# Optimization experiments

Measured on AMD Instinct MI355X. Metric: run time of the kernel, lower is better.

Reference implementation:

```python
import jax, jax.numpy as jnp
import numpy as np

N_NODES = 10000
N_EDGES = 640000
D_IN = 128
D_OUT = 128


def setup_inputs() -> dict:
    key = jax.random.key(0)
    k1, k2, k3, k4 = jax.random.split(key, 4)
    x = jax.random.normal(k1, (N_NODES, D_IN), dtype=jnp.float32)
    # PyG GCNConv weight: [dim_out, dim_in] (glorot)
    W = jax.random.normal(k2, (D_OUT, D_IN), dtype=jnp.float32) * (1.0 / np.sqrt(D_IN))
    b = jnp.zeros((D_OUT,), dtype=jnp.float32)
    edge_weight = jax.random.uniform(k3, (N_EDGES,), dtype=jnp.float32)
    edge_index = jax.random.randint(k4, (2, N_EDGES), 0, N_NODES, dtype=jnp.int32)
    return {"x": x, "W": W, "b": b, "edge_weight": edge_weight, "edge_index": edge_index}


def reference(x, W, b, edge_weight, edge_index):
    N = x.shape[0]
    # --- add self loops (fill weight = 1.0), PyG default ---
    loops = jnp.arange(N, dtype=edge_index.dtype)
    src = jnp.concatenate([edge_index[0], loops])
    dst = jnp.concatenate([edge_index[1], loops])
    ew = jnp.concatenate([edge_weight, jnp.ones((N,), dtype=edge_weight.dtype)])
    # --- symmetric GCN normalization: deg from target index ---
    deg = jax.ops.segment_sum(ew, dst, num_segments=N)
    dinv = jnp.where(deg > 0, jax.lax.rsqrt(deg), 0.0)
    norm = dinv[src] * ew * dinv[dst]  # [E+N]
    # --- linear transform then gather-scale-scatter aggregation ---
    h = x @ W.T  # [N, D_OUT]
    msgs = h[src] * norm[:, None]  # [E+N, D_OUT]
    out = jax.ops.segment_sum(msgs, dst, num_segments=N)
    return out + b
```

## Files before the change

kernel.cpp:

```cpp
#include <hip/hip_runtime.h>

#define N_NODES 10000
#define N_EDGES 640000
#define D 128
#define CAP 128

typedef unsigned long long ull;
typedef unsigned short u16;
typedef unsigned int u32;

#define CHUNKS 128
#define EPC 5000
#define GEMM_NPB 32
#define GEMM_BLOCKS ((N_NODES + GEMM_NPB - 1) / GEMM_NPB)
#define SMEM_BYTES 80000
#define FRACM 0xffffffffffffull

__device__ __forceinline__ u16 f2bf(float f) {
    unsigned u = __float_as_uint(f);
    unsigned r = (u + 0x7fffu + ((u >> 16) & 1u)) >> 16;
    return (u16)r;
}


__global__ void __launch_bounds__(256, 2) k_hist_fill_gemm(
    const int* __restrict__ src, const int* __restrict__ dst,
    const float* __restrict__ ew, ull* __restrict__ gpacked,
    const float* __restrict__ x, const float* __restrict__ W,
    u16* __restrict__ h_bf, ull* __restrict__ csr)
{
    extern __shared__ char smem[];
    const int t = threadIdx.x;

    if (blockIdx.x < CHUNKS) {
        ull* hist = (ull*)smem;
        for (int i = t; i < N_NODES; i += 256) hist[i] = 0;
        __syncthreads();

        const int e0 = blockIdx.x * EPC;
        u32 dlr[20];
        #pragma unroll
        for (int i = 0; i < 20; ++i) {
            int idx = i * 256 + t;
            dlr[i] = 0xffffffffu;
            if (idx < EPC) {
                int e = e0 + idx;
                int d = dst[e];
                ull add = (1ull << 48) | (ull)(ew[e] * 4294967296.0f);
                ull old = atomicAdd(&hist[d], add);
                dlr[i] = ((u32)d << 7) | (u32)((old >> 48) & 127u);
            }
        }
        __syncthreads();

        for (int i = t; i < N_NODES; i += 256) {
            ull v = hist[i];
            if (v) {
                ull old = atomicAdd(&gpacked[i], v);
                hist[i] = old >> 48;
            }
        }
        __syncthreads();

        #pragma unroll
        for (int i = 0; i < 20; ++i) {
            if (dlr[i] != 0xffffffffu) {
                int e = e0 + i * 256 + t;
                int d = (int)(dlr[i] >> 7);
                int lr = (int)(dlr[i] & 127u);
                int slot = (int)(u32)hist[d] + lr;
                csr[(size_t)d * CAP + slot] =
                    ((ull)__float_as_uint(ew[e]) << 32) | (unsigned)src[e];
            }
        }
    } else {
        float* xs = (float*)smem;
        const int gb = blockIdx.x - CHUNKS;
        const int node0 = gb * GEMM_NPB;
        const int col = t & 127;
        const int half = t >> 7;

        #pragma unroll
        for (int r = 0; r < 16; ++r) {
            int row = half * 16 + r;
            int n = node0 + row;
            xs[row * D + col] = (n < N_NODES) ? x[n * D + col] : 0.0f;
        }
        __syncthreads();

        float acc[16];
        #pragma unroll
        for (int r = 0; r < 16; ++r) acc[r] = 0.0f;

        const float4* Wrow = (const float4*)&W[col * D];
        const float* xbase = &xs[half * 16 * D];
        for (int k4 = 0; k4 < D / 4; ++k4) {
            float4 w = Wrow[k4];
            int k = k4 * 4;
            #pragma unroll
            for (int r = 0; r < 16; ++r) {
                acc[r] += xbase[r * D + k + 0] * w.x;
                acc[r] += xbase[r * D + k + 1] * w.y;
                acc[r] += xbase[r * D + k + 2] * w.z;
                acc[r] += xbase[r * D + k + 3] * w.w;
            }
        }
        #pragma unroll
        for (int r = 0; r < 16; ++r) {
            int n = node0 + half * 16 + r;
            if (n < N_NODES) h_bf[n * D + col] = f2bf(acc[r]);
        }
    }
}


__global__ void k_agg(const ull* __restrict__ gpacked, const ull* __restrict__ csr,
                      const u16* __restrict__ h_bf, const float* __restrict__ b,
                      float* __restrict__ out) {
    const int n = blockIdx.x;
    const int tid = threadIdx.x;
    const int jj = tid >> 4;
    const int lane = tid & 15;
    __shared__ int   ssrc[CAP];
    __shared__ float snm[CAP];
    __shared__ float4 red[128][2];

    const ull gp = gpacked[n];
    const int deg = (int)(gp >> 48);
    const float dn = rsqrtf(1.0f + (float)(gp & FRACM) * 0x1p-32f);
    const ull* bucket = csr + (size_t)n * CAP;

    if (tid < deg) {
        ull v = bucket[tid];
        int s = (int)(unsigned)(v & 0xffffffffu);
        float w = __uint_as_float((u32)(v >> 32));
        ull gs = gpacked[s];
        float ds_ = rsqrtf(1.0f + (float)(gs & FRACM) * 0x1p-32f);
        ssrc[tid] = s;
        snm[tid] = ds_ * w * dn;
    }
    __syncthreads();

    float acc[8];
    #pragma unroll
    for (int k = 0; k < 8; ++k) acc[k] = 0.0f;

    for (int j = jj; j < deg; j += 8) {
        int s = ssrc[j];
        float nm = snm[j];
        union { float4 f4; unsigned u[4]; } uu;
        uu.f4 = *(const float4*)(h_bf + (size_t)s * D + lane * 8);
        #pragma unroll
        for (int k = 0; k < 4; ++k) {
            acc[2 * k]     += __uint_as_float(uu.u[k] << 16) * nm;
            acc[2 * k + 1] += __uint_as_float(uu.u[k] & 0xffff0000u) * nm;
        }
    }
    red[tid][0] = make_float4(acc[0], acc[1], acc[2], acc[3]);
    red[tid][1] = make_float4(acc[4], acc[5], acc[6], acc[7]);
    __syncthreads();

    if (tid < 16) {
        float r0[8];
        #pragma unroll
        for (int k = 0; k < 8; ++k) r0[k] = 0.0f;
        #pragma unroll
        for (int s = 0; s < 8; ++s) {
            float4 a = red[s * 16 + tid][0];
            float4 c = red[s * 16 + tid][1];
            r0[0] += a.x; r0[1] += a.y; r0[2] += a.z; r0[3] += a.w;
            r0[4] += c.x; r0[5] += c.y; r0[6] += c.z; r0[7] += c.w;
        }
        float s2 = dn * dn;
        union { float4 f4; unsigned u[4]; } hh;
        hh.f4 = *(const float4*)(h_bf + (size_t)n * D + tid * 8);
        float hv[8];
        #pragma unroll
        for (int k = 0; k < 4; ++k) {
            hv[2 * k]     = __uint_as_float(hh.u[k] << 16);
            hv[2 * k + 1] = __uint_as_float(hh.u[k] & 0xffff0000u);
        }
        const float4* b4 = (const float4*)(b + tid * 8);
        float4 b0 = b4[0], b1 = b4[1];
        float4 o0, o1;
        o0.x = r0[0] + hv[0] * s2 + b0.x;
        o0.y = r0[1] + hv[1] * s2 + b0.y;
        o0.z = r0[2] + hv[2] * s2 + b0.z;
        o0.w = r0[3] + hv[3] * s2 + b0.w;
        o1.x = r0[4] + hv[4] * s2 + b1.x;
        o1.y = r0[5] + hv[5] * s2 + b1.y;
        o1.z = r0[6] + hv[6] * s2 + b1.z;
        o1.w = r0[7] + hv[7] * s2 + b1.w;
        float4* o4 = (float4*)(out + (size_t)n * D + tid * 8);
        o4[0] = o0;
        o4[1] = o1;
    }
}


extern "C" void kernel_launch(void* const* d_in, const int* in_sizes, int n_in,
                              void* d_out, int out_size, void* d_ws, size_t ws_size,
                              hipStream_t stream) {
    const float* x  = (const float*)d_in[0];
    const float* W  = (const float*)d_in[1];
    const float* b  = (const float*)d_in[2];
    const float* ew = (const float*)d_in[3];
    const int* ei   = (const int*)d_in[4];
    const int* src = ei;
    const int* dst = ei + N_EDGES;
    float* out = (float*)d_out;

    char* ws = (char*)d_ws;
    ull*   gpacked = (ull*)(ws);
    u16*   h_bf    = (u16*)(ws + 80000);
    ull*   csr     = (ull*)(ws + 2640000);

    hipMemsetAsync(gpacked, 0, 80000, stream);
    k_hist_fill_gemm<<<CHUNKS + GEMM_BLOCKS, 256, SMEM_BYTES, stream>>>(
        src, dst, ew, gpacked, x, W, h_bf, csr);
    k_agg<<<N_NODES, 128, 0, stream>>>(gpacked, csr, h_bf, b, out);
}
```

Baseline: 120.4 us.

## Use one wavefront per node in aggregation and stagger global histogram atomics

The aggregation kernel now assigns one 64-lane wavefront per destination node, with four nodes per 256-thread block. Each lane owns two output columns, which removes the shared-memory cross-thread reduction and one block barrier. Source indices and normalisation weights are packed into a single 64-bit shared entry. Separately, each histogram chunk starts its global atomic flush at a different node offset to reduce contention on the same addresses. The trade-off is narrower 4-byte gathers per lane instead of 16-byte ones, so each wave walks every neighbour serially.

```diff
diff --git a/kernel.cpp b/kernel.cpp
--- a/kernel.cpp
+++ b/kernel.cpp
@@ -53,7 +53,10 @@
         }
         __syncthreads();
 
-        for (int i = t; i < N_NODES; i += 256) {
+        const int off = blockIdx.x * (N_NODES / CHUNKS);
+        for (int ii = t; ii < N_NODES; ii += 256) {
+            int i = ii + off;
+            if (i >= N_NODES) i -= N_NODES;
             ull v = hist[i];
             if (v) {
                 ull old = atomicAdd(&gpacked[i], v);
@@ -114,87 +117,60 @@
 }
 
 
-__global__ void k_agg(const ull* __restrict__ gpacked, const ull* __restrict__ csr,
-                      const u16* __restrict__ h_bf, const float* __restrict__ b,
-                      float* __restrict__ out) {
-    const int n = blockIdx.x;
-    const int tid = threadIdx.x;
-    const int jj = tid >> 4;
-    const int lane = tid & 15;
-    __shared__ int   ssrc[CAP];
-    __shared__ float snm[CAP];
-    __shared__ float4 red[128][2];
+#define AGG_NPB 4
+
+__global__ void __launch_bounds__(256) k_agg(
+    const ull* __restrict__ gpacked, const ull* __restrict__ csr,
+    const u16* __restrict__ h_bf, const float* __restrict__ b,
+    float* __restrict__ out)
+{
+    const int wid  = threadIdx.x >> 6;
+    const int lane = threadIdx.x & 63;
+    const int n = blockIdx.x * AGG_NPB + wid;
+
+    __shared__ ull sm[AGG_NPB][CAP];
 
     const ull gp = gpacked[n];
     const int deg = (int)(gp >> 48);
     const float dn = rsqrtf(1.0f + (float)(gp & FRACM) * 0x1p-32f);
     const ull* bucket = csr + (size_t)n * CAP;
 
-    if (tid < deg) {
-        ull v = bucket[tid];
-        int s = (int)(unsigned)(v & 0xffffffffu);
-        float w = __uint_as_float((u32)(v >> 32));
-        ull gs = gpacked[s];
-        float ds_ = rsqrtf(1.0f + (float)(gs & FRACM) * 0x1p-32f);
-        ssrc[tid] = s;
-        snm[tid] = ds_ * w * dn;
+    #pragma unroll
+    for (int r = 0; r < 2; ++r) {
+        int j = r * 64 + lane;
+        if (j < deg) {
+            ull v = bucket[j];
+            int s = (int)(u32)(v & 0xffffffffu);
+            float w = __uint_as_float((u32)(v >> 32));
+            ull gs = gpacked[s];
+            float ds_ = rsqrtf(1.0f + (float)(gs & FRACM) * 0x1p-32f);
+            float nm = ds_ * w * dn;
+            sm[wid][j] = ((ull)__float_as_uint(nm) << 32) | (u32)s;
+        }
     }
     __syncthreads();
 
-    float acc[8];
-    #pragma unroll
-    for (int k = 0; k < 8; ++k) acc[k] = 0.0f;
+    float acc0 = 0.0f, acc1 = 0.0f;
+    const ull* smw = sm[wid];
+    #pragma unroll 4
+    for (int j = 0; j < deg; ++j) {
+        ull v = smw[j];
+        int s = (int)(u32)v;
+        float nm = __uint_as_float((u32)(v >> 32));
+        u32 hc = *(const u32*)(h_bf + (size_t)s * D + lane * 2);
+        acc0 += __uint_as_float(hc << 16) * nm;
+        acc1 += __uint_as_float(hc & 0xffff0000u) * nm;
+    }
 
-    for (int j = jj; j < deg; j += 8) {
-        int s = ssrc[j];
-        float nm = snm[j];
-        union { float4 f4; unsigned u[4]; } uu;
-        uu.f4 = *(const float4*)(h_bf + (size_t)s * D + lane * 8);
-        #pragma unroll
-        for (int k = 0; k < 4; ++k) {
-            acc[2 * k]     += __uint_as_float(uu.u[k] << 16) * nm;
-            acc[2 * k + 1] += __uint_as_float(uu.u[k] & 0xffff0000u) * nm;
-        }
-    }
-    red[tid][0] = make_float4(acc[0], acc[1], acc[2], acc[3]);
-    red[tid][1] = make_float4(acc[4], acc[5], acc[6], acc[7]);
-    __syncthreads();
-
-    if (tid < 16) {
-        float r0[8];
-        #pragma unroll
-        for (int k = 0; k < 8; ++k) r0[k] = 0.0f;
-        #pragma unroll
-        for (int s = 0; s < 8; ++s) {
-            float4 a = red[s * 16 + tid][0];
-            float4 c = red[s * 16 + tid][1];
-            r0[0] += a.x; r0[1] += a.y; r0[2] += a.z; r0[3] += a.w;
-            r0[4] += c.x; r0[5] += c.y; r0[6] += c.z; r0[7] += c.w;
-        }
-        float s2 = dn * dn;
-        union { float4 f4; unsigned u[4]; } hh;
-        hh.f4 = *(const float4*)(h_bf + (size_t)n * D + tid * 8);
-        float hv[8];
-        #pragma unroll
-        for (int k = 0; k < 4; ++k) {
-            hv[2 * k]     = __uint_as_float(hh.u[k] << 16);
-            hv[2 * k + 1] = __uint_as_float(hh.u[k] & 0xffff0000u);
-        }
-        const float4* b4 = (const float4*)(b + tid * 8);
-        float4 b0 = b4[0], b1 = b4[1];
-        float4 o0, o1;
-        o0.x = r0[0] + hv[0] * s2 + b0.x;
-        o0.y = r0[1] + hv[1] * s2 + b0.y;
-        o0.z = r0[2] + hv[2] * s2 + b0.z;
-        o0.w = r0[3] + hv[3] * s2 + b0.w;
-        o1.x = r0[4] + hv[4] * s2 + b1.x;
-        o1.y = r0[5] + hv[5] * s2 + b1.y;
-        o1.z = r0[6] + hv[6] * s2 + b1.z;
-        o1.w = r0[7] + hv[7] * s2 + b1.w;
-        float4* o4 = (float4*)(out + (size_t)n * D + tid * 8);
-        o4[0] = o0;
-        o4[1] = o1;
-    }
+    float s2 = dn * dn;
+    u32 hs = *(const u32*)(h_bf + (size_t)n * D + lane * 2);
+    acc0 += __uint_as_float(hs << 16) * s2;
+    acc1 += __uint_as_float(hs & 0xffff0000u) * s2;
+    float2 bb = *(const float2*)(b + lane * 2);
+    float2 o;
+    o.x = acc0 + bb.x;
+    o.y = acc1 + bb.y;
+    *(float2*)(out + (size_t)n * D + lane * 2) = o;
 }
 
 
@@ -218,5 +194,5 @@
     hipMemsetAsync(gpacked, 0, 80000, stream);
     k_hist_fill_gemm<<<CHUNKS + GEMM_BLOCKS, 256, SMEM_BYTES, stream>>>(
         src, dst, ew, gpacked, x, W, h_bf, csr);
-    k_agg<<<N_NODES, 128, 0, stream>>>(gpacked, csr, h_bf, b, out);
+    k_agg<<<N_NODES / AGG_NPB, 256, 0, stream>>>(gpacked, csr, h_bf, b, out);
 }
```

Result: no change. 120.8 us (+0.3%).
